# Kernel optimization log

Measured on AMD Instinct MI355X. Metric: run time of the kernel, lower is better.

The kernel has to match this reference:

```python
import jax, jax.numpy as jnp
import numpy as np
from jax import lax

DIM = 256; HEADS = 16; DHEAD = 16; H = 12; W = 26
DS = 4; KOFF = 6; OSCALE = 4.0
SCALE = DHEAD ** -0.5
EPS = 1e-5


def _create_grid(hh, ww, dtype):
    # channel0 = x (width index), channel1 = y (height index); matches torch meshgrid(arange(w), arange(h), indexing='xy')
    gy, gx = jnp.meshgrid(jnp.arange(hh, dtype=dtype), jnp.arange(ww, dtype=dtype), indexing='ij')
    return jnp.stack([gx, gy], axis=0)  # (2, hh, ww)


def _grid_sample_bilinear(img, grid):
    # F.grid_sample, mode='bilinear', padding_mode='zeros', align_corners=False
    # img (B,C,Hi,Wi); grid (B,Ho,Wo,2), grid[...,0]=x-norm, grid[...,1]=y-norm in [-1,1]
    B, C, Hi, Wi = img.shape
    x = ((grid[..., 0] + 1.0) * Wi - 1.0) / 2.0
    y = ((grid[..., 1] + 1.0) * Hi - 1.0) / 2.0
    x0 = jnp.floor(x); y0 = jnp.floor(y)

    def gather(xi, yi):
        valid = ((xi >= 0) & (xi < Wi) & (yi >= 0) & (yi < Hi)).astype(img.dtype)
        xc = jnp.clip(xi, 0, Wi - 1).astype(jnp.int32)
        yc = jnp.clip(yi, 0, Hi - 1).astype(jnp.int32)
        v = jax.vmap(lambda im, yy, xx: im[:, yy, xx])(img, yc, xc)  # (B,C,Ho,Wo)
        return v * valid[:, None]

    wx1 = (x - x0)[:, None]; wx0 = 1.0 - wx1
    wy1 = (y - y0)[:, None]; wy0 = 1.0 - wy1
    return (gather(x0, y0) * wy0 * wx0 + gather(x0 + 1.0, y0) * wy0 * wx1
            + gather(x0, y0 + 1.0) * wy1 * wx0 + gather(x0 + 1.0, y0 + 1.0) * wy1 * wx1)


def _forward(x, q, w_off_dw, b_off_dw, w_off_pw, wk, wv, w_out, b_out,
             cpb_w1, cpb_b1, cpb_w2, cpb_b2, cpb_w3, cpb_b3,
             conv1d_w, conv1d_b, ln_g, ln_b):
    b = x.shape[0]
    # faithful to torch: q.repeat(1,1,h*w).view(bs,1,dim,h,w).squeeze(1) == tile then reshape
    q_map = jnp.tile(q[:, 0, :], (1, H * W)).reshape(b, DIM, H, W)

    # to_offsets: depthwise Conv2d(k=6,s=4,p=1) -> GELU -> 1x1 conv (no bias) -> tanh -> *offset_scale
    t = lax.conv_general_dilated(q_map, w_off_dw, window_strides=(DS, DS),
                                 padding=[(1, 1), (1, 1)], feature_group_count=DIM,
                                 dimension_numbers=('NCHW', 'OIHW', 'NCHW'))
    t = jax.nn.gelu(t + b_off_dw[None, :, None, None], approximate=False)
    off = jnp.tanh(jnp.einsum('oc,bchw->bohw', w_off_pw, t)) * OSCALE  # (b,2,Hk,Wk)
    Hk, Wk = off.shape[-2], off.shape[-1]  # 3, 6

    gkv = _create_grid(Hk, Wk, x.dtype)
    vg0 = gkv[0] + off[:, 0]
    vg1 = gkv[1] + off[:, 1]
    # faithful repo normalize_grid: channel0 / (h-1), channel1 / (w-1)
    n0 = 2.0 * vg0 / max(Hk - 1, 1) - 1.0
    n1 = 2.0 * vg1 / max(Wk - 1, 1) - 1.0
    vgrid_scaled = jnp.stack([n0, n1], axis=-1)  # (b, Hk, Wk, 2)

    kv = _grid_sample_bilinear(x, vgrid_scaled)  # (b, DIM, Hk, Wk)
    k = jnp.einsum('oc,bchw->bohw', wk, kv)
    v = jnp.einsum('oc,bchw->bohw', wv, kv)

    qh = (q_map * SCALE).reshape(b, HEADS, DHEAD, H * W).transpose(0, 1, 3, 2)  # (b,h,i,d)
    kh = k.reshape(b, HEADS, DHEAD, Hk * Wk).transpose(0, 1, 3, 2)              # (b,h,j,d)
    vh = v.reshape(b, HEADS, DHEAD, Hk * Wk).transpose(0, 1, 3, 2)
    sim = jnp.einsum('bhid,bhjd->bhij', qh, kh)  # (b,16,312,18)

    # CPB relative position bias
    gq = _create_grid(H, W, x.dtype)
    gq0 = 2.0 * gq[0] / max(H - 1, 1) - 1.0
    gq1 = 2.0 * gq[1] / max(W - 1, 1) - 1.0
    grid_q = jnp.stack([gq0, gq1], axis=-1).reshape(1, H * W, 2)
    grid_kv = vgrid_scaled.reshape(b, Hk * Wk, 2)
    pos = grid_q[:, :, None, :] - grid_kv[:, None, :, :]       # (b,i,j,2)
    bias = jnp.sign(pos) * jnp.log(jnp.abs(pos) + 1.0)
    bias = jax.nn.relu(bias @ cpb_w1.T + cpb_b1)
    bias = jax.nn.relu(bias @ cpb_w2.T + cpb_b2)
    bias = bias @ cpb_w3.T + cpb_b3                             # (b,i,j,heads)
    sim = sim + bias.transpose(0, 3, 1, 2)

    attn = jax.nn.softmax(sim, axis=-1)  # dropout(0.1) identity in eval
    out = jnp.einsum('bhij,bhjd->bhid', attn, vh)               # (b,h,i,d)
    out = out.transpose(0, 1, 3, 2).reshape(b, DIM, H, W)        # 'b h (x y) d -> b (h d) x y'
    out = jnp.einsum('oc,bchw->bohw', w_out, out) + b_out[None, :, None, None]

    # SpatialCrossAttention tail: view -> permute -> Conv1d(312,1,1) -> residual -> LayerNorm
    tokens = out.reshape(b, DIM, H * W).transpose(0, 2, 1)       # (b,312,256)
    pooled = jnp.einsum('t,btc->bc', conv1d_w, tokens)[:, None, :] + conv1d_b[None, :, None]
    y = pooled + q
    mu = y.mean(-1, keepdims=True)
    var = y.var(-1, keepdims=True)
    return (y - mu) / jnp.sqrt(var + EPS) * ln_g + ln_b          # (b,1,256)


def setup_inputs() -> dict:
    key = jax.random.key(0)
    ks = jax.random.split(key, 16)
    rn = lambda i, shape, s=0.02: jax.random.normal(ks[i], shape, dtype=jnp.float32) * s
    B = 256
    return {
        'x': jax.random.normal(ks[0], (B, DIM, H, W), dtype=jnp.float32),
        'q': jax.random.normal(ks[1], (B, 1, DIM), dtype=jnp.float32),
        'w_off_dw': rn(2, (DIM, 1, KOFF, KOFF), 0.05),
        'b_off_dw': jnp.zeros((DIM,), jnp.float32),
        'w_off_pw': rn(3, (2, DIM), 0.05),
        'wk': rn(4, (DIM, DIM)),
        'wv': rn(5, (DIM, DIM)),
        'w_out': rn(6, (DIM, DIM)),
        'b_out': jnp.zeros((DIM,), jnp.float32),
        'cpb_w1': rn(7, (64, 2), 0.1),
        'cpb_b1': jnp.zeros((64,), jnp.float32),
        'cpb_w2': rn(8, (64, 64), 0.1),
        'cpb_b2': jnp.zeros((64,), jnp.float32),
        'cpb_w3': rn(9, (HEADS, 64), 0.1),
        'cpb_b3': jnp.zeros((HEADS,), jnp.float32),
        'conv1d_w': rn(10, (H * W,), 0.05),
        'conv1d_b': jnp.zeros((1,), jnp.float32),
        'ln_g': jnp.ones((DIM,), jnp.float32),
        'ln_b': jnp.zeros((DIM,), jnp.float32),
    }


def reference(x, q, w_off_dw, b_off_dw, w_off_pw, wk, wv, w_out, b_out,
              cpb_w1, cpb_b1, cpb_w2, cpb_b2, cpb_w3, cpb_b3,
              conv1d_w, conv1d_b, ln_g, ln_b):
    return _forward(x, q, w_off_dw, b_off_dw, w_off_pw, wk, wv, w_out, b_out,
                    cpb_w1, cpb_b1, cpb_w2, cpb_b2, cpb_w3, cpb_b3,
                    conv1d_w, conv1d_b, ln_g, ln_b)
```

## Files before the change

kernel.cpp:

```cpp
#include <hip/hip_runtime.h>
#include <hip/hip_bf16.h>
#include <math.h>


typedef __attribute__((ext_vector_type(8))) short short8;
typedef __attribute__((ext_vector_type(4))) float floatx4;

union U16 { uint4 u; short8 s; };

#define MFMA(A, B, C) __builtin_amdgcn_mfma_f32_16x16x32_bf16((A), (B), (C), 0, 0, 0)

__device__ __forceinline__ unsigned int f2bf(float f) {
    unsigned int u = __float_as_uint(f);
    u += 0x7fffu + ((u >> 16) & 1u);
    return u >> 16;
}
__device__ __forceinline__ unsigned int pk2(float a, float b) {
    __hip_bfloat162 h = __float22bfloat162_rn(make_float2(a, b));
    union { __hip_bfloat162 h; unsigned int u; } cv; cv.h = h;
    return cv.u;
}
__device__ __forceinline__ float bf2f(unsigned short v) {
    return __uint_as_float((unsigned int)v << 16);
}
__device__ __forceinline__ uint4 pack8(float4 a, float4 b) {
    uint4 r;
    r.x = pk2(a.x, a.y); r.y = pk2(a.z, a.w);
    r.z = pk2(b.x, b.y); r.w = pk2(b.z, b.w);
    return r;
}

__global__ __launch_bounds__(512, 2) void k_all(
    const float* __restrict__ x, const float* __restrict__ q,
    const float* __restrict__ w_dw, const float* __restrict__ b_dw,
    const float* __restrict__ w_pw,
    const float* __restrict__ wk, const float* __restrict__ wv,
    const float* __restrict__ w_out, const float* __restrict__ b_out,
    const float* __restrict__ cw1, const float* __restrict__ cb1,
    const float* __restrict__ cw2, const float* __restrict__ cb2,
    const float* __restrict__ cw3, const float* __restrict__ cb3,
    const float* __restrict__ conv_w, const float* __restrict__ conv_b,
    const float* __restrict__ ln_g, const float* __restrict__ ln_b,
    float* __restrict__ out)
{
    const int b = blockIdx.x, tid = threadIdx.x;
    const int w = tid >> 6, lane = tid & 63;
    const int n = lane & 15, qd = lane >> 4;

    __shared__ float qf_s[256];
    __shared__ unsigned short q_sb[256];
    __shared__ unsigned short v_sb[5120];
    __shared__ float F0[468], F1[216];
    __shared__ unsigned int lutxy[312];
    __shared__ float off_s[36], n0_s[18], n1_s[18];
    __shared__ float sx0[18], sy0[18], swx[18], swy[18];
    __shared__ float b2_s[64], b3_s[16];
    __shared__ float wA_s[288];
    __shared__ __align__(16) float m_s[256];
    __shared__ float pooled_s[256], redb[24];
    __shared__ __align__(16) unsigned char UB[113152];
    float* Sbuf = (float*)UB;
    unsigned short* kvT = (unsigned short*)UB;
    float* qsw = (float*)UB;
    float* t_s = (float*)(UB + 16512);
    unsigned short* k_sb = (unsigned short*)(UB + 16512);
    unsigned int* h2w = (unsigned int*)(UB + 78336);
    float* wred = (float*)UB;

    uint4 W2f[4][2], W3f[2];
    {
        const float4* cw2_4 = (const float4*)cw2;
        #pragma unroll
        for (int mtl = 0; mtl < 4; ++mtl)
            #pragma unroll
            for (int ks = 0; ks < 2; ++ks) {
                const int base = (mtl * 16 + n) * 16 + ks * 8 + qd * 2;
                W2f[mtl][ks] = pack8(cw2_4[base], cw2_4[base + 1]);
            }
        const float4* cw3_4 = (const float4*)cw3;
        #pragma unroll
        for (int ks = 0; ks < 2; ++ks) {
            const int base = n * 16 + ks * 8 + qd * 2;
            W3f[ks] = pack8(cw3_4[base], cw3_4[base + 1]);
        }
    }
    float W1a[16], W1b[16], B1r[16];
    #pragma unroll
    for (int kk = 0; kk < 16; ++kk) {
        const int kid = (kk < 8) ? (qd * 8 + kk) : (32 + qd * 8 + kk - 8);
        W1a[kk] = cw1[kid * 2]; W1b[kk] = cw1[kid * 2 + 1]; B1r[kk] = cb1[kid];
    }

    if (tid < 256) {
        const float qv = q[b * 256 + tid];
        qf_s[tid] = qv;
        q_sb[tid] = (unsigned short)f2bf(qv * 0.25f);
    }
    for (int u = tid; u < 4128; u += 512) {
        const int r = u / 258, i = u - r * 258;
        qsw[u] = (i < 256) ? q[b * 256 + i] : 0.f;
    }
    if (tid < 312) {
        const int iy = tid / 26;
        lutxy[tid] = (unsigned int)(tid - iy * 26) | ((unsigned int)iy << 16);
    }
    if (tid < 64) b2_s[tid] = cb2[tid];
    if (tid < 16) b3_s[tid] = cb3[tid];
    __syncthreads();

    {
        const int c = tid & 255, g = tid >> 8;
        float wreg[36];
        const float4* wdw4 = (const float4*)w_dw;
        #pragma unroll
        for (int i = 0; i < 9; ++i) {
            const float4 t4 = wdw4[c * 9 + i];
            wreg[i * 4 + 0] = t4.x; wreg[i * 4 + 1] = t4.y;
            wreg[i * 4 + 2] = t4.z; wreg[i * 4 + 3] = t4.w;
        }
        float acc[9];
        const float bv = b_dw[c];
        #pragma unroll
        for (int a = 0; a < 9; ++a) acc[a] = bv;
        const int cb = (c * 56) & 255;
        const int cp = (c & 15) * 258;
        for (int jh = 0; jh < 3; ++jh) {
            for (int kh = 0; kh < 6; ++kh) {
                const int ih = jh * 4 - 1 + kh;
                if (ih < 0 || ih >= 12) continue;
                const int rb = ih * 26;
                #pragma unroll
                for (int jwl = 0; jwl < 3; ++jwl) {
                    const int jw = g * 3 + jwl;
                    #pragma unroll
                    for (int kw = 0; kw < 6; ++kw) {
                        const int iw = jw * 4 - 1 + kw;
                        if (iw < 0 || iw >= 26) continue;
                        acc[jh * 3 + jwl] += wreg[kh * 6 + kw] * qsw[cp + ((cb + rb + iw) & 255)];
                    }
                }
            }
        }
        #pragma unroll
        for (int a = 0; a < 9; ++a) {
            const int jh = a / 3, jwl = a - jh * 3;
            const int p = jh * 6 + g * 3 + jwl;
            const float v = acc[a];
            t_s[p * 256 + c] = 0.5f * v * (1.0f + erff(v * 0.70710678118654752f));
        }
    }
    __syncthreads();

    for (int oi = w; oi < 36; oi += 8) {
        const int o = oi / 18, p = oi - o * 18;
        float s = 0.f;
        for (int c = lane; c < 256; c += 64) s += w_pw[o * 256 + c] * t_s[p * 256 + c];
        for (int d = 32; d > 0; d >>= 1) s += __shfl_down(s, d, 64);
        if (lane == 0) off_s[oi] = 4.0f * tanhf(s);
    }
    __syncthreads();

    if (tid < 18) {
        const int j = tid, jh = j / 6, jw = j - jh * 6;
        const float vg0 = (float)jw + off_s[j];
        const float vg1 = (float)jh + off_s[18 + j];
        const float n0 = 2.0f * vg0 / 2.0f - 1.0f;
        const float n1 = 2.0f * vg1 / 5.0f - 1.0f;
        n0_s[j] = n0; n1_s[j] = n1;
        const float xp = ((n0 + 1.0f) * 26.0f - 1.0f) * 0.5f;
        const float yp = ((n1 + 1.0f) * 12.0f - 1.0f) * 0.5f;
        const float x0 = floorf(xp), y0 = floorf(yp);
        sx0[j] = x0; sy0[j] = y0; swx[j] = xp - x0; swy[j] = yp - y0;
    }
    __syncthreads();

    {
        const int c = tid & 255, g = tid >> 8;
        const float* xb = x + ((size_t)b * 256 + c) * 312;
        for (int jj = 0; jj < 9; ++jj) {
            const int j = g * 9 + jj;
            const int x0 = (int)sx0[j], y0 = (int)sy0[j];
            const int x1 = x0 + 1, y1 = y0 + 1;
            const float wx1 = swx[j], wy1 = swy[j];
            const float wx0 = 1.f - wx1, wy0 = 1.f - wy1;
            const bool xv0 = (x0 >= 0) & (x0 < 26), xv1 = (x1 >= 0) & (x1 < 26);
            const bool yv0 = (y0 >= 0) & (y0 < 12), yv1 = (y1 >= 0) & (y1 < 12);
            const float v00 = (xv0 & yv0) ? xb[y0 * 26 + x0] : 0.f;
            const float v01 = (xv1 & yv0) ? xb[y0 * 26 + x1] : 0.f;
            const float v10 = (xv0 & yv1) ? xb[y1 * 26 + x0] : 0.f;
            const float v11 = (xv1 & yv1) ? xb[y1 * 26 + x1] : 0.f;
            const float val = wy0 * (wx0 * v00 + wx1 * v01) + wy1 * (wx0 * v10 + wx1 * v11);
            kvT[j * 264 + c] = (unsigned short)f2bf(val);
        }
    }
    for (int u = tid; u < 684; u += 512) {
        if (u < 468) {
            const int ixv = u / 18, j = u - ixv * 18;
            const float p0 = (float)ixv * (2.0f / 11.0f) - 1.0f - n0_s[j];
            F0[u] = copysignf(__logf(1.0f + fabsf(p0)), p0);
        } else {
            const int u2 = u - 468;
            const int iyv = u2 / 18, j = u2 - iyv * 18;
            const float p1 = (float)iyv * (2.0f / 25.0f) - 1.0f - n1_s[j];
            F1[u2] = copysignf(__logf(1.0f + fabsf(p1)), p1);
        }
    }
    __syncthreads();

    {
        const int m2 = w & 1, mtb = w >> 1;
        const float4* wm4 = (const float4*)(m2 ? wv : wk);
        floatx4 pa[4][2];
        #pragma unroll
        for (int a = 0; a < 4; ++a) {
            pa[a][0] = (floatx4){0.f, 0.f, 0.f, 0.f};
            pa[a][1] = (floatx4){0.f, 0.f, 0.f, 0.f};
        }
        #pragma unroll 2
        for (int ks = 0; ks < 8; ++ks) {
            U16 b0, b1;
            b0.u = *(const uint4*)(kvT + n * 264 + ks * 32 + qd * 8);
            b1.u = make_uint4(0u, 0u, 0u, 0u);
            if (n < 2) b1.u = *(const uint4*)(kvT + (16 + n) * 264 + ks * 32 + qd * 8);
            #pragma unroll
            for (int mtl = 0; mtl < 4; ++mtl) {
                const int mt = mtb + mtl * 4;
                const int f4i = (mt * 16 + n) * 64 + ks * 8 + qd * 2;
                U16 A; A.u = pack8(wm4[f4i], wm4[f4i + 1]);
                pa[mtl][0] = MFMA(A.s, b0.s, pa[mtl][0]);
                pa[mtl][1] = MFMA(A.s, b1.s, pa[mtl][1]);
            }
        }
        unsigned short* dst = m2 ? v_sb : k_sb;
        #pragma unroll
        for (int mtl = 0; mtl < 4; ++mtl) {
            const int mt = mtb + mtl * 4;
            #pragma unroll
            for (int r = 0; r < 4; ++r) {
                const int o = mt * 16 + qd * 4 + r;
                dst[o * 20 + n] = (unsigned short)f2bf(pa[mtl][0][r]);
                if (n < 2) dst[o * 20 + 16 + n] = (unsigned short)f2bf(pa[mtl][1][r]);
            }
        }
    }
    __syncthreads();

    uint4 BkU[2][2];
    #pragma unroll
    for (int hh = 0; hh < 2; ++hh)
        #pragma unroll
        for (int jt = 0; jt < 2; ++jt) {
            unsigned int u0 = 0, u1 = 0, u2 = 0, u3 = 0;
            if (qd < 2 && (jt == 0 || n < 2)) {
                const int h = w * 2 + hh;
                const int j = jt * 16 + n;
                const int cb0 = (h * 16 + qd * 8) * 20 + j;
                u0 = (unsigned)k_sb[cb0] | ((unsigned)k_sb[cb0 + 20] << 16);
                u1 = (unsigned)k_sb[cb0 + 40] | ((unsigned)k_sb[cb0 + 60] << 16);
                u2 = (unsigned)k_sb[cb0 + 80] | ((unsigned)k_sb[cb0 + 100] << 16);
                u3 = (unsigned)k_sb[cb0 + 120] | ((unsigned)k_sb[cb0 + 140] << 16);
            }
            BkU[hh][jt] = make_uint4(u0, u1, u2, u3);
        }
    __syncthreads();

    float wAcc[18];
    #pragma unroll
    for (int j = 0; j < 18; ++j) wAcc[j] = 0.f;

    auto soft_acc = [&](int chp, const float* Sp) {
        const int il = tid >> 4, h = tid & 15;
        const int CIp = (chp == 9) ? 24 : 32;
        if (il < CIp) {
            const float cwv = conv_w[chp * 32 + il];
            float lv[18];
            #pragma unroll
            for (int j = 0; j < 18; ++j) lv[j] = Sp[(il * 18 + j) * 17 + h];
            float m = lv[0];
            #pragma unroll
            for (int j = 1; j < 18; ++j) m = fmaxf(m, lv[j]);
            float s = 0.f;
            #pragma unroll
            for (int j = 0; j < 18; ++j) { lv[j] = __expf(lv[j] - m); s += lv[j]; }
            const float wgt = cwv / s;
            #pragma unroll
            for (int j = 0; j < 18; ++j) wAcc[j] = fmaf(wgt, lv[j], wAcc[j]);
        }
    };

    for (int ch = 0; ch < 10; ++ch) {
        float* Sc = Sbuf + (ch & 1) * 9792;
        const float* Sp = Sbuf + ((ch & 1) ^ 1) * 9792;
        const int ibase = ch * 32;

        #pragma unroll
        for (int hh = 0; hh < 2; ++hh) {
            const int h = w * 2 + hh;
            const int base = h * 16 + qd * 8;
            #pragma unroll
            for (int ig = 0; ig < 2; ++ig) {
                unsigned int a0 = 0, a1 = 0, a2 = 0, a3u = 0;
                if (qd < 2) {
                    const int ii = ibase + ig * 16 + n;
                    a0 = (unsigned)q_sb[((base + 0) * 56 + ii) & 255] |
                         ((unsigned)q_sb[((base + 1) * 56 + ii) & 255] << 16);
                    a1 = (unsigned)q_sb[((base + 2) * 56 + ii) & 255] |
                         ((unsigned)q_sb[((base + 3) * 56 + ii) & 255] << 16);
                    a2 = (unsigned)q_sb[((base + 4) * 56 + ii) & 255] |
                         ((unsigned)q_sb[((base + 5) * 56 + ii) & 255] << 16);
                    a3u = (unsigned)q_sb[((base + 6) * 56 + ii) & 255] |
                          ((unsigned)q_sb[((base + 7) * 56 + ii) & 255] << 16);
                }
                U16 Af; Af.u = make_uint4(a0, a1, a2, a3u);
                #pragma unroll
                for (int jt = 0; jt < 2; ++jt) {
                    U16 Bf; Bf.u = BkU[hh][jt];
                    floatx4 D = {0.f, 0.f, 0.f, 0.f};
                    D = MFMA(Af.s, Bf.s, D);
                    const int j = jt * 16 + n;
                    if (j < 18) {
                        #pragma unroll
                        for (int r = 0; r < 4; ++r)
                            Sc[((ig * 16 + qd * 4 + r) * 18 + j) * 17 + h] = D[r];
                    }
                }
            }
        }
        if (ch > 0) soft_acc(ch - 1, Sp);
        __syncthreads();

        {
            auto mlp2 = [&](int tA, int tB, bool two) {
                const int tv2[2] = {tA, tB};
                U16 ub0[2], ub1[2];
                #pragma unroll
                for (int u2 = 0; u2 < 2; ++u2) {
                    const int t = tv2[u2];
                    const int ig = (t >= 18) ? 1 : 0;
                    const int j = t - ig * 18;
                    const int i0 = ibase + ig * 16 + n;
                    const unsigned int lv2 = lutxy[(i0 < 312) ? i0 : 311];
                    const int ix = (int)(lv2 & 0xffffu), iy = (int)(lv2 >> 16);
                    const float f0 = F0[ix * 18 + j];
                    const float f1 = F1[iy * 18 + j];
                    unsigned int uu[8];
                    #pragma unroll
                    for (int kp = 0; kp < 8; ++kp) {
                        const float ha = fmaxf(fmaf(W1a[2*kp],   f0, fmaf(W1b[2*kp],   f1, B1r[2*kp])),   0.f);
                        const float hb = fmaxf(fmaf(W1a[2*kp+1], f0, fmaf(W1b[2*kp+1], f1, B1r[2*kp+1])), 0.f);
                        uu[kp] = pk2(ha, hb);
                    }
                    ub0[u2].u = make_uint4(uu[0], uu[1], uu[2], uu[3]);
                    ub1[u2].u = make_uint4(uu[4], uu[5], uu[6], uu[7]);
                }
                #pragma unroll
                for (int u2 = 0; u2 < 2; ++u2) {
                    if (u2 == 1 && !two) break;
                    unsigned int* hw = h2w + ((w << 1) | u2) * 544 + n * 34;
                    #pragma unroll
                    for (int mtl = 0; mtl < 4; ++mtl) {
                        U16 A0, A1; A0.u = W2f[mtl][0]; A1.u = W2f[mtl][1];
                        floatx4 acc = {0.f, 0.f, 0.f, 0.f};
                        acc = MFMA(A0.s, ub0[u2].s, acc);
                        acc = MFMA(A1.s, ub1[u2].s, acc);
                        const float e0 = fmaxf(acc[0] + b2_s[mtl*16 + qd*4 + 0], 0.f);
                        const float e1 = fmaxf(acc[1] + b2_s[mtl*16 + qd*4 + 1], 0.f);
                        const float e2 = fmaxf(acc[2] + b2_s[mtl*16 + qd*4 + 2], 0.f);
                        const float e3 = fmaxf(acc[3] + b2_s[mtl*16 + qd*4 + 3], 0.f);
                        hw[mtl * 8 + qd * 2]     = pk2(e0, e1);
                        hw[mtl * 8 + qd * 2 + 1] = pk2(e2, e3);
                    }
                }
                #pragma unroll
                for (int u2 = 0; u2 < 2; ++u2) {
                    if (u2 == 1 && !two) break;
                    const unsigned int* hwr = h2w + ((w << 1) | u2) * 544;
                    U16 uc0, uc1;
                    uc0.u = *(const uint4*)(hwr + n * 34 + qd * 4);
                    uc1.u = *(const uint4*)(hwr + n * 34 + 16 + qd * 4);
                    U16 A0, A1; A0.u = W3f[0]; A1.u = W3f[1];
                    floatx4 a3 = {0.f, 0.f, 0.f, 0.f};
                    a3 = MFMA(A0.s, uc0.s, a3);
                    a3 = MFMA(A1.s, uc1.s, a3);
                    const int t = tv2[u2];
                    const int ig = (t >= 18) ? 1 : 0;
                    const int j = t - ig * 18;
                    float* sp = Sc + ((ig * 16 + n) * 18 + j) * 17 + qd * 4;
                    #pragma unroll
                    for (int r = 0; r < 4; ++r) sp[r] = a3[r] + b3_s[qd * 4 + r] + sp[r];
                }
            };
            mlp2(w, w + 8, true);
            mlp2(w + 16, w + 24, true);
            if (w < 4) mlp2(32 + w, 32 + w, false);
        }
        __syncthreads();
    }
    soft_acc(9, Sbuf + 9792);

    #pragma unroll
    for (int j = 0; j < 18; ++j) wred[tid * 18 + j] = wAcc[j];
    {
        float v = 0.f;
        for (int u = tid; u < 312; u += 512) v += conv_w[u];
        for (int d = 32; d > 0; d >>= 1) v += __shfl_down(v, d, 64);
        if (lane == 0) redb[w] = v;
    }
    __syncthreads();
    for (int u = tid; u < 288; u += 512) {
        const int h = u / 18, j = u - h * 18;
        float s = 0.f;
        #pragma unroll
        for (int sl = 0; sl < 32; ++sl) s += wred[(sl * 16 + h) * 18 + j];
        wA_s[u] = s;
    }
    __syncthreads();

    if (tid < 256) {
        const int hb = (tid >> 4) * 18;
        float acc = 0.f;
        #pragma unroll
        for (int j = 0; j < 18; ++j) acc += wA_s[hb + j] * bf2f(v_sb[tid * 20 + j]);
        m_s[tid] = acc;
    }
    __syncthreads();

    float Ssum = 0.f;
    #pragma unroll
    for (int i = 0; i < 8; ++i) Ssum += redb[i];

    {
        const float4 mm = *(const float4*)(m_s + lane * 4);
        for (int ol = 0; ol < 32; ++ol) {
            const int o = w * 32 + ol;
            const float4 wq = *(const float4*)(w_out + o * 256 + lane * 4);
            float d = wq.x * mm.x + wq.y * mm.y + wq.z * mm.z + wq.w * mm.w;
            for (int dd = 32; dd > 0; dd >>= 1) d += __shfl_down(d, dd, 64);
            if (lane == 0) pooled_s[o] = d;
        }
    }
    __syncthreads();

    if (tid < 256) {
        const float y = pooled_s[tid] + b_out[tid] * Ssum + conv_b[0] + qf_s[tid];
        float s1 = y, s2 = y * y;
        for (int d = 32; d > 0; d >>= 1) { s1 += __shfl_down(s1, d, 64); s2 += __shfl_down(s2, d, 64); }
        if (lane == 0) { redb[16 + w] = s1; redb[20 + w] = s2; }
    }
    __syncthreads();
    if (tid < 256) {
        const float y = pooled_s[tid] + b_out[tid] * Ssum + conv_b[0] + qf_s[tid];
        const float S1 = redb[16] + redb[17] + redb[18] + redb[19];
        const float S2 = redb[20] + redb[21] + redb[22] + redb[23];
        const float mu = S1 * (1.0f / 256.0f);
        const float var = S2 * (1.0f / 256.0f) - mu * mu;
        out[b * 256 + tid] = (y - mu) * rsqrtf(var + 1e-5f) * ln_g[tid] + ln_b[tid];
    }
}

extern "C" void kernel_launch(void* const* d_in, const int* in_sizes, int n_in,
                              void* d_out, int out_size, void* d_ws, size_t ws_size,
                              hipStream_t stream) {
    const float* x       = (const float*)d_in[0];
    const float* q       = (const float*)d_in[1];
    const float* w_dw    = (const float*)d_in[2];
    const float* b_dwp   = (const float*)d_in[3];
    const float* w_pw    = (const float*)d_in[4];
    const float* wk      = (const float*)d_in[5];
    const float* wv      = (const float*)d_in[6];
    const float* w_out   = (const float*)d_in[7];
    const float* b_out   = (const float*)d_in[8];
    const float* cw1     = (const float*)d_in[9];
    const float* cb1     = (const float*)d_in[10];
    const float* cw2     = (const float*)d_in[11];
    const float* cb2     = (const float*)d_in[12];
    const float* cw3     = (const float*)d_in[13];
    const float* cb3     = (const float*)d_in[14];
    const float* conv_w  = (const float*)d_in[15];
    const float* conv_b  = (const float*)d_in[16];
    const float* ln_g    = (const float*)d_in[17];
    const float* ln_b    = (const float*)d_in[18];
    float* out = (float*)d_out;

    k_all<<<256, 512, 0, stream>>>(x, q, w_dw, b_dwp, w_pw, wk, wv, w_out, b_out,
                                   cw1, cb1, cw2, cb2, cw3, cb3,
                                   conv_w, conv_b, ln_g, ln_b, out);
}
```

Before: 261.2 us.

## Double block size to 1024 threads and redistribute per-wave work

Launches 1024 threads per block instead of 512 and re-splits every phase: depthwise conv positions, grid sampling, K/V projection tiles, one head per wave in the score MFMA, single-token MLP per call, and softmax split across two lanes with shuffle reductions. It also moves the MLP weight register loads to later in the kernel, which shortens their live range. The goal is more waves per block to hide latency and fewer serial iterations per thread. The cost is one block per CU instead of two, plus extra shuffles and barrier cost across more waves.

```diff
diff --git a/kernel.cpp b/kernel.cpp
--- a/kernel.cpp
+++ b/kernel.cpp
@@ -30,7 +30,7 @@
     return r;
 }
 
-__global__ __launch_bounds__(512, 2) void k_all(
+__global__ __launch_bounds__(1024, 1) void k_all(
     const float* __restrict__ x, const float* __restrict__ q,
     const float* __restrict__ w_dw, const float* __restrict__ b_dw,
     const float* __restrict__ w_pw,
@@ -67,36 +67,12 @@
     unsigned int* h2w = (unsigned int*)(UB + 78336);
     float* wred = (float*)UB;
 
-    uint4 W2f[4][2], W3f[2];
-    {
-        const float4* cw2_4 = (const float4*)cw2;
-        #pragma unroll
-        for (int mtl = 0; mtl < 4; ++mtl)
-            #pragma unroll
-            for (int ks = 0; ks < 2; ++ks) {
-                const int base = (mtl * 16 + n) * 16 + ks * 8 + qd * 2;
-                W2f[mtl][ks] = pack8(cw2_4[base], cw2_4[base + 1]);
-            }
-        const float4* cw3_4 = (const float4*)cw3;
-        #pragma unroll
-        for (int ks = 0; ks < 2; ++ks) {
-            const int base = n * 16 + ks * 8 + qd * 2;
-            W3f[ks] = pack8(cw3_4[base], cw3_4[base + 1]);
-        }
-    }
-    float W1a[16], W1b[16], B1r[16];
-    #pragma unroll
-    for (int kk = 0; kk < 16; ++kk) {
-        const int kid = (kk < 8) ? (qd * 8 + kk) : (32 + qd * 8 + kk - 8);
-        W1a[kk] = cw1[kid * 2]; W1b[kk] = cw1[kid * 2 + 1]; B1r[kk] = cb1[kid];
-    }
-
     if (tid < 256) {
         const float qv = q[b * 256 + tid];
         qf_s[tid] = qv;
         q_sb[tid] = (unsigned short)f2bf(qv * 0.25f);
     }
-    for (int u = tid; u < 4128; u += 512) {
+    for (int u = tid; u < 4128; u += 1024) {
         const int r = u / 258, i = u - r * 258;
         qsw[u] = (i < 256) ? q[b * 256 + i] : 0.f;
     }
@@ -118,40 +94,35 @@
             wreg[i * 4 + 0] = t4.x; wreg[i * 4 + 1] = t4.y;
             wreg[i * 4 + 2] = t4.z; wreg[i * 4 + 3] = t4.w;
         }
-        float acc[9];
         const float bv = b_dw[c];
-        #pragma unroll
-        for (int a = 0; a < 9; ++a) acc[a] = bv;
         const int cb = (c * 56) & 255;
         const int cp = (c & 15) * 258;
-        for (int jh = 0; jh < 3; ++jh) {
-            for (int kh = 0; kh < 6; ++kh) {
-                const int ih = jh * 4 - 1 + kh;
-                if (ih < 0 || ih >= 12) continue;
-                const int rb = ih * 26;
+        #pragma unroll
+        for (int it = 0; it < 5; ++it) {
+            const int p = g + it * 4;
+            if (p < 18) {
+                const int jh = (p >= 12) ? 2 : ((p >= 6) ? 1 : 0);
+                const int jw = p - jh * 6;
+                float acc = bv;
                 #pragma unroll
-                for (int jwl = 0; jwl < 3; ++jwl) {
-                    const int jw = g * 3 + jwl;
+                for (int kh = 0; kh < 6; ++kh) {
+                    const int ih = jh * 4 - 1 + kh;
+                    if (ih < 0 || ih >= 12) continue;
+                    const int rb = ih * 26;
                     #pragma unroll
                     for (int kw = 0; kw < 6; ++kw) {
                         const int iw = jw * 4 - 1 + kw;
                         if (iw < 0 || iw >= 26) continue;
-                        acc[jh * 3 + jwl] += wreg[kh * 6 + kw] * qsw[cp + ((cb + rb + iw) & 255)];
+                        acc += wreg[kh * 6 + kw] * qsw[cp + ((cb + rb + iw) & 255)];
                     }
                 }
-            }
-        }
-        #pragma unroll
-        for (int a = 0; a < 9; ++a) {
-            const int jh = a / 3, jwl = a - jh * 3;
-            const int p = jh * 6 + g * 3 + jwl;
-            const float v = acc[a];
-            t_s[p * 256 + c] = 0.5f * v * (1.0f + erff(v * 0.70710678118654752f));
-        }
-    }
-    __syncthreads();
-
-    for (int oi = w; oi < 36; oi += 8) {
+                t_s[p * 256 + c] = 0.5f * acc * (1.0f + erff(acc * 0.70710678118654752f));
+            }
+        }
+    }
+    __syncthreads();
+
+    for (int oi = w; oi < 36; oi += 16) {
         const int o = oi / 18, p = oi - o * 18;
         float s = 0.f;
         for (int c = lane; c < 256; c += 64) s += w_pw[o * 256 + c] * t_s[p * 256 + c];
@@ -177,23 +148,26 @@
     {
         const int c = tid & 255, g = tid >> 8;
         const float* xb = x + ((size_t)b * 256 + c) * 312;
-        for (int jj = 0; jj < 9; ++jj) {
-            const int j = g * 9 + jj;
-            const int x0 = (int)sx0[j], y0 = (int)sy0[j];
-            const int x1 = x0 + 1, y1 = y0 + 1;
-            const float wx1 = swx[j], wy1 = swy[j];
-            const float wx0 = 1.f - wx1, wy0 = 1.f - wy1;
-            const bool xv0 = (x0 >= 0) & (x0 < 26), xv1 = (x1 >= 0) & (x1 < 26);
-            const bool yv0 = (y0 >= 0) & (y0 < 12), yv1 = (y1 >= 0) & (y1 < 12);
-            const float v00 = (xv0 & yv0) ? xb[y0 * 26 + x0] : 0.f;
-            const float v01 = (xv1 & yv0) ? xb[y0 * 26 + x1] : 0.f;
-            const float v10 = (xv0 & yv1) ? xb[y1 * 26 + x0] : 0.f;
-            const float v11 = (xv1 & yv1) ? xb[y1 * 26 + x1] : 0.f;
-            const float val = wy0 * (wx0 * v00 + wx1 * v01) + wy1 * (wx0 * v10 + wx1 * v11);
-            kvT[j * 264 + c] = (unsigned short)f2bf(val);
-        }
-    }
-    for (int u = tid; u < 684; u += 512) {
+        #pragma unroll
+        for (int jj = 0; jj < 5; ++jj) {
+            const int j = g + jj * 4;
+            if (j < 18) {
+                const int x0 = (int)sx0[j], y0 = (int)sy0[j];
+                const int x1 = x0 + 1, y1 = y0 + 1;
+                const float wx1 = swx[j], wy1 = swy[j];
+                const float wx0 = 1.f - wx1, wy0 = 1.f - wy1;
+                const bool xv0 = (x0 >= 0) & (x0 < 26), xv1 = (x1 >= 0) & (x1 < 26);
+                const bool yv0 = (y0 >= 0) & (y0 < 12), yv1 = (y1 >= 0) & (y1 < 12);
+                const float v00 = (xv0 & yv0) ? xb[y0 * 26 + x0] : 0.f;
+                const float v01 = (xv1 & yv0) ? xb[y0 * 26 + x1] : 0.f;
+                const float v10 = (xv0 & yv1) ? xb[y1 * 26 + x0] : 0.f;
+                const float v11 = (xv1 & yv1) ? xb[y1 * 26 + x1] : 0.f;
+                const float val = wy0 * (wx0 * v00 + wx1 * v01) + wy1 * (wx0 * v10 + wx1 * v11);
+                kvT[j * 264 + c] = (unsigned short)f2bf(val);
+            }
+        }
+    }
+    for (int u = tid; u < 684; u += 1024) {
         if (u < 468) {
             const int ixv = u / 18, j = u - ixv * 18;
             const float p0 = (float)ixv * (2.0f / 11.0f) - 1.0f - n0_s[j];
@@ -210,9 +184,9 @@
     {
         const int m2 = w & 1, mtb = w >> 1;
         const float4* wm4 = (const float4*)(m2 ? wv : wk);
-        floatx4 pa[4][2];
-        #pragma unroll
-        for (int a = 0; a < 4; ++a) {
+        floatx4 pa[2][2];
+        #pragma unroll
+        for (int a = 0; a < 2; ++a) {
             pa[a][0] = (floatx4){0.f, 0.f, 0.f, 0.f};
             pa[a][1] = (floatx4){0.f, 0.f, 0.f, 0.f};
         }
@@ -223,8 +197,8 @@
             b1.u = make_uint4(0u, 0u, 0u, 0u);
             if (n < 2) b1.u = *(const uint4*)(kvT + (16 + n) * 264 + ks * 32 + qd * 8);
             #pragma unroll
-            for (int mtl = 0; mtl < 4; ++mtl) {
-                const int mt = mtb + mtl * 4;
+            for (int mtl = 0; mtl < 2; ++mtl) {
+                const int mt = mtb + mtl * 8;
                 const int f4i = (mt * 16 + n) * 64 + ks * 8 + qd * 2;
                 U16 A; A.u = pack8(wm4[f4i], wm4[f4i + 1]);
                 pa[mtl][0] = MFMA(A.s, b0.s, pa[mtl][0]);
@@ -233,8 +207,8 @@
         }
         unsigned short* dst = m2 ? v_sb : k_sb;
         #pragma unroll
-        for (int mtl = 0; mtl < 4; ++mtl) {
-            const int mt = mtb + mtl * 4;
+        for (int mtl = 0; mtl < 2; ++mtl) {
+            const int mt = mtb + mtl * 8;
             #pragma unroll
             for (int r = 0; r < 4; ++r) {
                 const int o = mt * 16 + qd * 4 + r;
@@ -245,46 +219,70 @@
     }
     __syncthreads();
 
-    uint4 BkU[2][2];
+    uint4 W2f[4][2], W3f[2];
+    {
+        const float4* cw2_4 = (const float4*)cw2;
+        #pragma unroll
+        for (int mtl = 0; mtl < 4; ++mtl)
+            #pragma unroll
+            for (int ks = 0; ks < 2; ++ks) {
+                const int base = (mtl * 16 + n) * 16 + ks * 8 + qd * 2;
+                W2f[mtl][ks] = pack8(cw2_4[base], cw2_4[base + 1]);
+            }
+        const float4* cw3_4 = (const float4*)cw3;
+        #pragma unroll
+        for (int ks = 0; ks < 2; ++ks) {
+            const int base = n * 16 + ks * 8 + qd * 2;
+            W3f[ks] = pack8(cw3_4[base], cw3_4[base + 1]);
+        }
+    }
+    float W1a[16], W1b[16], B1r[16];
     #pragma unroll
-    for (int hh = 0; hh < 2; ++hh)
-        #pragma unroll
-        for (int jt = 0; jt < 2; ++jt) {
-            unsigned int u0 = 0, u1 = 0, u2 = 0, u3 = 0;
-            if (qd < 2 && (jt == 0 || n < 2)) {
-                const int h = w * 2 + hh;
-                const int j = jt * 16 + n;
-                const int cb0 = (h * 16 + qd * 8) * 20 + j;
-                u0 = (unsigned)k_sb[cb0] | ((unsigned)k_sb[cb0 + 20] << 16);
-                u1 = (unsigned)k_sb[cb0 + 40] | ((unsigned)k_sb[cb0 + 60] << 16);
-                u2 = (unsigned)k_sb[cb0 + 80] | ((unsigned)k_sb[cb0 + 100] << 16);
-                u3 = (unsigned)k_sb[cb0 + 120] | ((unsigned)k_sb[cb0 + 140] << 16);
-            }
-            BkU[hh][jt] = make_uint4(u0, u1, u2, u3);
-        }
-    __syncthreads();
-
-    float wAcc[18];
+    for (int kk = 0; kk < 16; ++kk) {
+        const int kid = (kk < 8) ? (qd * 8 + kk) : (32 + qd * 8 + kk - 8);
+        W1a[kk] = cw1[kid * 2]; W1b[kk] = cw1[kid * 2 + 1]; B1r[kk] = cb1[kid];
+    }
+
+    uint4 BkU[2];
     #pragma unroll
-    for (int j = 0; j < 18; ++j) wAcc[j] = 0.f;
+    for (int jt = 0; jt < 2; ++jt) {
+        unsigned int u0 = 0, u1 = 0, u2 = 0, u3 = 0;
+        if (qd < 2 && (jt == 0 || n < 2)) {
+            const int j = jt * 16 + n;
+            const int cb0 = (w * 16 + qd * 8) * 20 + j;
+            u0 = (unsigned)k_sb[cb0] | ((unsigned)k_sb[cb0 + 20] << 16);
+            u1 = (unsigned)k_sb[cb0 + 40] | ((unsigned)k_sb[cb0 + 60] << 16);
+            u2 = (unsigned)k_sb[cb0 + 80] | ((unsigned)k_sb[cb0 + 100] << 16);
+            u3 = (unsigned)k_sb[cb0 + 120] | ((unsigned)k_sb[cb0 + 140] << 16);
+        }
+        BkU[jt] = make_uint4(u0, u1, u2, u3);
+    }
+    __syncthreads();
+
+    float wAcc[9];
+    #pragma unroll
+    for (int jl = 0; jl < 9; ++jl) wAcc[jl] = 0.f;
 
     auto soft_acc = [&](int chp, const float* Sp) {
-        const int il = tid >> 4, h = tid & 15;
+        const int h = tid & 15, hf = (tid >> 4) & 1, il = tid >> 5;
         const int CIp = (chp == 9) ? 24 : 32;
         if (il < CIp) {
             const float cwv = conv_w[chp * 32 + il];
-            float lv[18];
-            #pragma unroll
-            for (int j = 0; j < 18; ++j) lv[j] = Sp[(il * 18 + j) * 17 + h];
+            float lv[9];
+            const float* row = Sp + (il * 18 + hf * 9) * 17 + h;
+            #pragma unroll
+            for (int jl = 0; jl < 9; ++jl) lv[jl] = row[jl * 17];
             float m = lv[0];
             #pragma unroll
-            for (int j = 1; j < 18; ++j) m = fmaxf(m, lv[j]);
+            for (int jl = 1; jl < 9; ++jl) m = fmaxf(m, lv[jl]);
+            m = fmaxf(m, __shfl_xor(m, 16, 64));
             float s = 0.f;
             #pragma unroll
-            for (int j = 0; j < 18; ++j) { lv[j] = __expf(lv[j] - m); s += lv[j]; }
+            for (int jl = 0; jl < 9; ++jl) { lv[jl] = __expf(lv[jl] - m); s += lv[jl]; }
+            s += __shfl_xor(s, 16, 64);
             const float wgt = cwv / s;
             #pragma unroll
-            for (int j = 0; j < 18; ++j) wAcc[j] = fmaf(wgt, lv[j], wAcc[j]);
+            for (int jl = 0; jl < 9; ++jl) wAcc[jl] = fmaf(wgt, lv[jl], wAcc[jl]);
         }
     };
 
@@ -293,10 +291,8 @@
         const float* Sp = Sbuf + ((ch & 1) ^ 1) * 9792;
         const int ibase = ch * 32;
 
-        #pragma unroll
-        for (int hh = 0; hh < 2; ++hh) {
-            const int h = w * 2 + hh;
-            const int base = h * 16 + qd * 8;
+        {
+            const int base = w * 16 + qd * 8;
             #pragma unroll
             for (int ig = 0; ig < 2; ++ig) {
                 unsigned int a0 = 0, a1 = 0, a2 = 0, a3u = 0;
@@ -314,14 +310,14 @@
                 U16 Af; Af.u = make_uint4(a0, a1, a2, a3u);
                 #pragma unroll
                 for (int jt = 0; jt < 2; ++jt) {
-                    U16 Bf; Bf.u = BkU[hh][jt];
+                    U16 Bf; Bf.u = BkU[jt];
                     floatx4 D = {0.f, 0.f, 0.f, 0.f};
                     D = MFMA(Af.s, Bf.s, D);
                     const int j = jt * 16 + n;
                     if (j < 18) {
                         #pragma unroll
                         for (int r = 0; r < 4; ++r)
-                            Sc[((ig * 16 + qd * 4 + r) * 18 + j) * 17 + h] = D[r];
+                            Sc[((ig * 16 + qd * 4 + r) * 18 + j) * 17 + w] = D[r];
                     }
                 }
             }
@@ -330,19 +326,16 @@
         __syncthreads();
 
         {
-            auto mlp2 = [&](int tA, int tB, bool two) {
-                const int tv2[2] = {tA, tB};
-                U16 ub0[2], ub1[2];
-                #pragma unroll
-                for (int u2 = 0; u2 < 2; ++u2) {
-                    const int t = tv2[u2];
-                    const int ig = (t >= 18) ? 1 : 0;
-                    const int j = t - ig * 18;
-                    const int i0 = ibase + ig * 16 + n;
-                    const unsigned int lv2 = lutxy[(i0 < 312) ? i0 : 311];
-                    const int ix = (int)(lv2 & 0xffffu), iy = (int)(lv2 >> 16);
-                    const float f0 = F0[ix * 18 + j];
-                    const float f1 = F1[iy * 18 + j];
+            auto mlp1 = [&](int t) {
+                const int ig = (t >= 18) ? 1 : 0;
+                const int j = t - ig * 18;
+                const int i0 = ibase + ig * 16 + n;
+                const unsigned int lv2 = lutxy[(i0 < 312) ? i0 : 311];
+                const int ix = (int)(lv2 & 0xffffu), iy = (int)(lv2 >> 16);
+                const float f0 = F0[ix * 18 + j];
+                const float f1 = F1[iy * 18 + j];
+                U16 ub0, ub1;
+                {
                     unsigned int uu[8];
                     #pragma unroll
                     for (int kp = 0; kp < 8; ++kp) {
@@ -350,69 +343,59 @@
                         const float hb = fmaxf(fmaf(W1a[2*kp+1], f0, fmaf(W1b[2*kp+1], f1, B1r[2*kp+1])), 0.f);
                         uu[kp] = pk2(ha, hb);
                     }
-                    ub0[u2].u = make_uint4(uu[0], uu[1], uu[2], uu[3]);
-                    ub1[u2].u = make_uint4(uu[4], uu[5], uu[6], uu[7]);
+                    ub0.u = make_uint4(uu[0], uu[1], uu[2], uu[3]);
+                    ub1.u = make_uint4(uu[4], uu[5], uu[6], uu[7]);
                 }
+                unsigned int* hw = h2w + w * 544 + n * 34;
                 #pragma unroll
-                for (int u2 = 0; u2 < 2; ++u2) {
-                    if (u2 == 1 && !two) break;
-                    unsigned int* hw = h2w + ((w << 1) | u2) * 544 + n * 34;
-                    #pragma unroll
-                    for (int mtl = 0; mtl < 4; ++mtl) {
-                        U16 A0, A1; A0.u = W2f[mtl][0]; A1.u = W2f[mtl][1];
-                        floatx4 acc = {0.f, 0.f, 0.f, 0.f};
-                        acc = MFMA(A0.s, ub0[u2].s, acc);
-                        acc = MFMA(A1.s, ub1[u2].s, acc);
-                        const float e0 = fmaxf(acc[0] + b2_s[mtl*16 + qd*4 + 0], 0.f);
-                        const float e1 = fmaxf(acc[1] + b2_s[mtl*16 + qd*4 + 1], 0.f);
-                        const float e2 = fmaxf(acc[2] + b2_s[mtl*16 + qd*4 + 2], 0.f);
-                        const float e3 = fmaxf(acc[3] + b2_s[mtl*16 + qd*4 + 3], 0.f);
-                        hw[mtl * 8 + qd * 2]     = pk2(e0, e1);
-                        hw[mtl * 8 + qd * 2 + 1] = pk2(e2, e3);
-                    }
+                for (int mtl = 0; mtl < 4; ++mtl) {
+                    U16 A0, A1; A0.u = W2f[mtl][0]; A1.u = W2f[mtl][1];
+                    floatx4 acc = {0.f, 0.f, 0.f, 0.f};
+                    acc = MFMA(A0.s, ub0.s, acc);
+                    acc = MFMA(A1.s, ub1.s, acc);
+                    const float e0 = fmaxf(acc[0] + b2_s[mtl*16 + qd*4 + 0], 0.f);
+                    const float e1 = fmaxf(acc[1] + b2_s[mtl*16 + qd*4 + 1], 0.f);
+                    const float e2 = fmaxf(acc[2] + b2_s[mtl*16 + qd*4 + 2], 0.f);
+                    const float e3 = fmaxf(acc[3] + b2_s[mtl*16 + qd*4 + 3], 0.f);
+                    hw[mtl * 8 + qd * 2]     = pk2(e0, e1);
+                    hw[mtl * 8 + qd * 2 + 1] = pk2(e2, e3);
                 }
+                const unsigned int* hwr = h2w + w * 544;
+                U16 uc0, uc1;
+                uc0.u = *(const uint4*)(hwr + n * 34 + qd * 4);
+                uc1.u = *(const uint4*)(hwr + n * 34 + 16 + qd * 4);
+                U16 A0, A1; A0.u = W3f[0]; A1.u = W3f[1];
+                floatx4 a3 = {0.f, 0.f, 0.f, 0.f};
+                a3 = MFMA(A0.s, uc0.s, a3);
+                a3 = MFMA(A1.s, uc1.s, a3);
+                float* sp = Sc + ((ig * 16 + n) * 18 + j) * 17 + qd * 4;
                 #pragma unroll
-                for (int u2 = 0; u2 < 2; ++u2) {
-                    if (u2 == 1 && !two) break;
-                    const unsigned int* hwr = h2w + ((w << 1) | u2) * 544;
-                    U16 uc0, uc1;
-                    uc0.u = *(const uint4*)(hwr + n * 34 + qd * 4);
-                    uc1.u = *(const uint4*)(hwr + n * 34 + 16 + qd * 4);
-                    U16 A0, A1; A0.u = W3f[0]; A1.u = W3f[1];
-                    floatx4 a3 = {0.f, 0.f, 0.f, 0.f};
-                    a3 = MFMA(A0.s, uc0.s, a3);
-                    a3 = MFMA(A1.s, uc1.s, a3);
-                    const int t = tv2[u2];
-                    const int ig = (t >= 18) ? 1 : 0;
-                    const int j = t - ig * 18;
-                    float* sp = Sc + ((ig * 16 + n) * 18 + j) * 17 + qd * 4;
-                    #pragma unroll
-                    for (int r = 0; r < 4; ++r) sp[r] = a3[r] + b3_s[qd * 4 + r] + sp[r];
-                }
+                for (int r = 0; r < 4; ++r) sp[r] = a3[r] + b3_s[qd * 4 + r] + sp[r];
             };
-            mlp2(w, w + 8, true);
-            mlp2(w + 16, w + 24, true);
-            if (w < 4) mlp2(32 + w, 32 + w, false);
+            mlp1(w);
+            mlp1(w + 16);
+            if (w < 4) mlp1(32 + w);
         }
         __syncthreads();
     }
     soft_acc(9, Sbuf + 9792);
 
     #pragma unroll
-    for (int j = 0; j < 18; ++j) wred[tid * 18 + j] = wAcc[j];
+    for (int jl = 0; jl < 9; ++jl) wred[tid * 9 + jl] = wAcc[jl];
     {
         float v = 0.f;
-        for (int u = tid; u < 312; u += 512) v += conv_w[u];
+        for (int u = tid; u < 312; u += 1024) v += conv_w[u];
         for (int d = 32; d > 0; d >>= 1) v += __shfl_down(v, d, 64);
         if (lane == 0) redb[w] = v;
     }
     __syncthreads();
-    for (int u = tid; u < 288; u += 512) {
-        const int h = u / 18, j = u - h * 18;
+    if (tid < 288) {
+        const int h = tid / 18, j2 = tid - h * 18;
+        const int hf = (j2 >= 9) ? 1 : 0, jl = j2 - hf * 9;
         float s = 0.f;
         #pragma unroll
-        for (int sl = 0; sl < 32; ++sl) s += wred[(sl * 16 + h) * 18 + j];
-        wA_s[u] = s;
+        for (int sl = 0; sl < 32; ++sl) s += wred[(sl * 32 + hf * 16 + h) * 9 + jl];
+        wA_s[tid] = s;
     }
     __syncthreads();
 
@@ -427,12 +410,12 @@
 
     float Ssum = 0.f;
     #pragma unroll
-    for (int i = 0; i < 8; ++i) Ssum += redb[i];
+    for (int i = 0; i < 16; ++i) Ssum += redb[i];
 
     {
         const float4 mm = *(const float4*)(m_s + lane * 4);
-        for (int ol = 0; ol < 32; ++ol) {
-            const int o = w * 32 + ol;
+        for (int ol = 0; ol < 16; ++ol) {
+            const int o = w * 16 + ol;
             const float4 wq = *(const float4*)(w_out + o * 256 + lane * 4);
             float d = wq.x * mm.x + wq.y * mm.y + wq.z * mm.z + wq.w * mm.w;
             for (int dd = 32; dd > 0; dd >>= 1) d += __shfl_down(d, dd, 64);
@@ -482,7 +465,7 @@
     const float* ln_b    = (const float*)d_in[18];
     float* out = (float*)d_out;
 
-    k_all<<<256, 512, 0, stream>>>(x, q, w_dw, b_dwp, w_pw, wk, wv, w_out, b_out,
-                                   cw1, cb1, cw2, cb2, cw3, cb3,
-                                   conv_w, conv_b, ln_g, ln_b, out);
-}
+    k_all<<<256, 1024, 0, stream>>>(x, q, w_dw, b_dwp, w_pw, wk, wv, w_out, b_out,
+                                    cw1, cb1, cw2, cb2, cw3, cb3,
+                                    conv_w, conv_b, ln_g, ln_b, out);
+}
```

Result: slower. 382.5 us (+46.5%).

## Pipeline score, MLP bias and softmax stages over triple-buffered chunks

Applied to the files above, without the earlier changes.

Restructures the per-chunk loop into a three-stage software pipeline (QK MFMA, CPB MLP bias add, softmax accumulation) using three score buffers, so each iteration needs only one barrier instead of two. The first-layer MLP weights move from per-thread registers into a packed shared table, and the W2/W3 fragment loads are deferred until after the projection phase, both to reduce register pressure. The MLP now processes one position at a time with a single h2w scratch per wave. Shared memory grows to hold the third buffer, which may limit occupancy, and the MLP loses its two-position batching.

```diff
diff --git a/kernel.cpp b/kernel.cpp
--- a/kernel.cpp
+++ b/kernel.cpp
@@ -55,41 +55,18 @@
     __shared__ float off_s[36], n0_s[18], n1_s[18];
     __shared__ float sx0[18], sy0[18], swx[18], swy[18];
     __shared__ float b2_s[64], b3_s[16];
+    __shared__ __align__(16) float w1p[4][8][8];
     __shared__ float wA_s[288];
     __shared__ __align__(16) float m_s[256];
     __shared__ float pooled_s[256], redb[24];
-    __shared__ __align__(16) unsigned char UB[113152];
+    __shared__ __align__(16) unsigned char UB[134912];
     float* Sbuf = (float*)UB;
     unsigned short* kvT = (unsigned short*)UB;
     float* qsw = (float*)UB;
     float* t_s = (float*)(UB + 16512);
     unsigned short* k_sb = (unsigned short*)(UB + 16512);
-    unsigned int* h2w = (unsigned int*)(UB + 78336);
-    float* wred = (float*)UB;
-
-    uint4 W2f[4][2], W3f[2];
-    {
-        const float4* cw2_4 = (const float4*)cw2;
-        #pragma unroll
-        for (int mtl = 0; mtl < 4; ++mtl)
-            #pragma unroll
-            for (int ks = 0; ks < 2; ++ks) {
-                const int base = (mtl * 16 + n) * 16 + ks * 8 + qd * 2;
-                W2f[mtl][ks] = pack8(cw2_4[base], cw2_4[base + 1]);
-            }
-        const float4* cw3_4 = (const float4*)cw3;
-        #pragma unroll
-        for (int ks = 0; ks < 2; ++ks) {
-            const int base = n * 16 + ks * 8 + qd * 2;
-            W3f[ks] = pack8(cw3_4[base], cw3_4[base + 1]);
-        }
-    }
-    float W1a[16], W1b[16], B1r[16];
-    #pragma unroll
-    for (int kk = 0; kk < 16; ++kk) {
-        const int kid = (kk < 8) ? (qd * 8 + kk) : (32 + qd * 8 + kk - 8);
-        W1a[kk] = cw1[kid * 2]; W1b[kk] = cw1[kid * 2 + 1]; B1r[kk] = cb1[kid];
-    }
+    unsigned int* h2w = (unsigned int*)(UB + 117504);
+    float* wred = (float*)(UB + 39168);
 
     if (tid < 256) {
         const float qv = q[b * 256 + tid];
@@ -106,6 +83,19 @@
     }
     if (tid < 64) b2_s[tid] = cb2[tid];
     if (tid < 16) b3_s[tid] = cb3[tid];
+    if (tid >= 64 && tid < 96) {
+        const int t2 = tid - 64;
+        const int qdi = t2 >> 3, kp = t2 & 7;
+        const int kk0 = 2 * kp, kk1 = 2 * kp + 1;
+        const int kid0 = (kk0 < 8) ? (qdi * 8 + kk0) : (32 + qdi * 8 + kk0 - 8);
+        const int kid1 = (kk1 < 8) ? (qdi * 8 + kk1) : (32 + qdi * 8 + kk1 - 8);
+        w1p[qdi][kp][0] = cw1[kid0 * 2];
+        w1p[qdi][kp][1] = cw1[kid0 * 2 + 1];
+        w1p[qdi][kp][2] = cb1[kid0];
+        w1p[qdi][kp][3] = cw1[kid1 * 2];
+        w1p[qdi][kp][4] = cw1[kid1 * 2 + 1];
+        w1p[qdi][kp][5] = cb1[kid1];
+    }
     __syncthreads();
 
     {
@@ -245,6 +235,24 @@
     }
     __syncthreads();
 
+    uint4 W2f[4][2], W3f[2];
+    {
+        const float4* cw2_4 = (const float4*)cw2;
+        #pragma unroll
+        for (int mtl = 0; mtl < 4; ++mtl)
+            #pragma unroll
+            for (int ks = 0; ks < 2; ++ks) {
+                const int base = (mtl * 16 + n) * 16 + ks * 8 + qd * 2;
+                W2f[mtl][ks] = pack8(cw2_4[base], cw2_4[base + 1]);
+            }
+        const float4* cw3_4 = (const float4*)cw3;
+        #pragma unroll
+        for (int ks = 0; ks < 2; ++ks) {
+            const int base = n * 16 + ks * 8 + qd * 2;
+            W3f[ks] = pack8(cw3_4[base], cw3_4[base + 1]);
+        }
+    }
+
     uint4 BkU[2][2];
     #pragma unroll
     for (int hh = 0; hh < 2; ++hh)
@@ -274,8 +282,9 @@
         if (il < CIp) {
             const float cwv = conv_w[chp * 32 + il];
             float lv[18];
-            #pragma unroll
-            for (int j = 0; j < 18; ++j) lv[j] = Sp[(il * 18 + j) * 17 + h];
+            const float* row = Sp + (il * 18) * 17 + h;
+            #pragma unroll
+            for (int j = 0; j < 18; ++j) lv[j] = row[j * 17];
             float m = lv[0];
             #pragma unroll
             for (int j = 1; j < 18; ++j) m = fmaxf(m, lv[j]);
@@ -288,115 +297,104 @@
         }
     };
 
-    for (int ch = 0; ch < 10; ++ch) {
-        float* Sc = Sbuf + (ch & 1) * 9792;
-        const float* Sp = Sbuf + ((ch & 1) ^ 1) * 9792;
-        const int ibase = ch * 32;
-
-        #pragma unroll
-        for (int hh = 0; hh < 2; ++hh) {
-            const int h = w * 2 + hh;
-            const int base = h * 16 + qd * 8;
-            #pragma unroll
-            for (int ig = 0; ig < 2; ++ig) {
-                unsigned int a0 = 0, a1 = 0, a2 = 0, a3u = 0;
-                if (qd < 2) {
-                    const int ii = ibase + ig * 16 + n;
-                    a0 = (unsigned)q_sb[((base + 0) * 56 + ii) & 255] |
-                         ((unsigned)q_sb[((base + 1) * 56 + ii) & 255] << 16);
-                    a1 = (unsigned)q_sb[((base + 2) * 56 + ii) & 255] |
-                         ((unsigned)q_sb[((base + 3) * 56 + ii) & 255] << 16);
-                    a2 = (unsigned)q_sb[((base + 4) * 56 + ii) & 255] |
-                         ((unsigned)q_sb[((base + 5) * 56 + ii) & 255] << 16);
-                    a3u = (unsigned)q_sb[((base + 6) * 56 + ii) & 255] |
-                          ((unsigned)q_sb[((base + 7) * 56 + ii) & 255] << 16);
-                }
-                U16 Af; Af.u = make_uint4(a0, a1, a2, a3u);
+    for (int t = 0; t < 12; ++t) {
+        if (t < 10) {
+            float* Sc = Sbuf + (t % 3) * 9792;
+            const int ibase = t * 32;
+            #pragma unroll
+            for (int hh = 0; hh < 2; ++hh) {
+                const int h = w * 2 + hh;
+                const int base = h * 16 + qd * 8;
                 #pragma unroll
-                for (int jt = 0; jt < 2; ++jt) {
-                    U16 Bf; Bf.u = BkU[hh][jt];
-                    floatx4 D = {0.f, 0.f, 0.f, 0.f};
-                    D = MFMA(Af.s, Bf.s, D);
-                    const int j = jt * 16 + n;
-                    if (j < 18) {
-                        #pragma unroll
-                        for (int r = 0; r < 4; ++r)
-                            Sc[((ig * 16 + qd * 4 + r) * 18 + j) * 17 + h] = D[r];
+                for (int ig = 0; ig < 2; ++ig) {
+                    unsigned int a0 = 0, a1 = 0, a2 = 0, a3u = 0;
+                    if (qd < 2) {
+                        const int ii = ibase + ig * 16 + n;
+                        a0 = (unsigned)q_sb[((base + 0) * 56 + ii) & 255] |
+                             ((unsigned)q_sb[((base + 1) * 56 + ii) & 255] << 16);
+                        a1 = (unsigned)q_sb[((base + 2) * 56 + ii) & 255] |
+                             ((unsigned)q_sb[((base + 3) * 56 + ii) & 255] << 16);
+                        a2 = (unsigned)q_sb[((base + 4) * 56 + ii) & 255] |
+                             ((unsigned)q_sb[((base + 5) * 56 + ii) & 255] << 16);
+                        a3u = (unsigned)q_sb[((base + 6) * 56 + ii) & 255] |
+                              ((unsigned)q_sb[((base + 7) * 56 + ii) & 255] << 16);
+                    }
+                    U16 Af; Af.u = make_uint4(a0, a1, a2, a3u);
+                    #pragma unroll
+                    for (int jt = 0; jt < 2; ++jt) {
+                        U16 Bf; Bf.u = BkU[hh][jt];
+                        floatx4 D = {0.f, 0.f, 0.f, 0.f};
+                        D = MFMA(Af.s, Bf.s, D);
+                        const int j = jt * 16 + n;
+                        if (j < 18) {
+                            #pragma unroll
+                            for (int r = 0; r < 4; ++r)
+                                Sc[((ig * 16 + qd * 4 + r) * 18 + j) * 17 + h] = D[r];
+                        }
                     }
                 }
             }
         }
-        if (ch > 0) soft_acc(ch - 1, Sp);
-        __syncthreads();
-
-        {
-            auto mlp2 = [&](int tA, int tB, bool two) {
-                const int tv2[2] = {tA, tB};
-                U16 ub0[2], ub1[2];
-                #pragma unroll
-                for (int u2 = 0; u2 < 2; ++u2) {
-                    const int t = tv2[u2];
-                    const int ig = (t >= 18) ? 1 : 0;
-                    const int j = t - ig * 18;
-                    const int i0 = ibase + ig * 16 + n;
-                    const unsigned int lv2 = lutxy[(i0 < 312) ? i0 : 311];
-                    const int ix = (int)(lv2 & 0xffffu), iy = (int)(lv2 >> 16);
-                    const float f0 = F0[ix * 18 + j];
-                    const float f1 = F1[iy * 18 + j];
+        if (t >= 1 && t < 11) {
+            const int chm = t - 1;
+            float* Sm = Sbuf + (chm % 3) * 9792;
+            const int ibase = chm * 32;
+            auto mlp1 = [&](int tt) {
+                const int ig = (tt >= 18) ? 1 : 0;
+                const int j = tt - ig * 18;
+                const int i0 = ibase + ig * 16 + n;
+                const unsigned int lv2 = lutxy[(i0 < 312) ? i0 : 311];
+                const int ix = (int)(lv2 & 0xffffu), iy = (int)(lv2 >> 16);
+                const float f0 = F0[ix * 18 + j];
+                const float f1 = F1[iy * 18 + j];
+                U16 ub0, ub1;
+                {
                     unsigned int uu[8];
                     #pragma unroll
                     for (int kp = 0; kp < 8; ++kp) {
-                        const float ha = fmaxf(fmaf(W1a[2*kp],   f0, fmaf(W1b[2*kp],   f1, B1r[2*kp])),   0.f);
-                        const float hb = fmaxf(fmaf(W1a[2*kp+1], f0, fmaf(W1b[2*kp+1], f1, B1r[2*kp+1])), 0.f);
+                        const float* wp = &w1p[qd][kp][0];
+                        const float ha = fmaxf(fmaf(wp[0], f0, fmaf(wp[1], f1, wp[2])), 0.f);
+                        const float hb = fmaxf(fmaf(wp[3], f0, fmaf(wp[4], f1, wp[5])), 0.f);
                         uu[kp] = pk2(ha, hb);
                     }
-                    ub0[u2].u = make_uint4(uu[0], uu[1], uu[2], uu[3]);
-                    ub1[u2].u = make_uint4(uu[4], uu[5], uu[6], uu[7]);
+                    ub0.u = make_uint4(uu[0], uu[1], uu[2], uu[3]);
+                    ub1.u = make_uint4(uu[4], uu[5], uu[6], uu[7]);
                 }
+                unsigned int* hw = h2w + w * 544 + n * 34;
                 #pragma unroll
-                for (int u2 = 0; u2 < 2; ++u2) {
-                    if (u2 == 1 && !two) break;
-                    unsigned int* hw = h2w + ((w << 1) | u2) * 544 + n * 34;
-                    #pragma unroll
-                    for (int mtl = 0; mtl < 4; ++mtl) {
-                        U16 A0, A1; A0.u = W2f[mtl][0]; A1.u = W2f[mtl][1];
-                        floatx4 acc = {0.f, 0.f, 0.f, 0.f};
-                        acc = MFMA(A0.s, ub0[u2].s, acc);
-                        acc = MFMA(A1.s, ub1[u2].s, acc);
-                        const float e0 = fmaxf(acc[0] + b2_s[mtl*16 + qd*4 + 0], 0.f);
-                        const float e1 = fmaxf(acc[1] + b2_s[mtl*16 + qd*4 + 1], 0.f);
-                        const float e2 = fmaxf(acc[2] + b2_s[mtl*16 + qd*4 + 2], 0.f);
-                        const float e3 = fmaxf(acc[3] + b2_s[mtl*16 + qd*4 + 3], 0.f);
-                        hw[mtl * 8 + qd * 2]     = pk2(e0, e1);
-                        hw[mtl * 8 + qd * 2 + 1] = pk2(e2, e3);
-                    }
+                for (int mtl = 0; mtl < 4; ++mtl) {
+                    U16 A0, A1; A0.u = W2f[mtl][0]; A1.u = W2f[mtl][1];
+                    floatx4 acc = {0.f, 0.f, 0.f, 0.f};
+                    acc = MFMA(A0.s, ub0.s, acc);
+                    acc = MFMA(A1.s, ub1.s, acc);
+                    const float e0 = fmaxf(acc[0] + b2_s[mtl*16 + qd*4 + 0], 0.f);
+                    const float e1 = fmaxf(acc[1] + b2_s[mtl*16 + qd*4 + 1], 0.f);
+                    const float e2 = fmaxf(acc[2] + b2_s[mtl*16 + qd*4 + 2], 0.f);
+                    const float e3 = fmaxf(acc[3] + b2_s[mtl*16 + qd*4 + 3], 0.f);
+                    hw[mtl * 8 + qd * 2]     = pk2(e0, e1);
+                    hw[mtl * 8 + qd * 2 + 1] = pk2(e2, e3);
                 }
+                const unsigned int* hwr = h2w + w * 544;
+                U16 uc0, uc1;
+                uc0.u = *(const uint4*)(hwr + n * 34 + qd * 4);
+                uc1.u = *(const uint4*)(hwr + n * 34 + 16 + qd * 4);
+                U16 A0, A1; A0.u = W3f[0]; A1.u = W3f[1];
+                floatx4 a3 = {0.f, 0.f, 0.f, 0.f};
+                a3 = MFMA(A0.s, uc0.s, a3);
+                a3 = MFMA(A1.s, uc1.s, a3);
+                float* sp = Sm + ((ig * 16 + n) * 18 + j) * 17 + qd * 4;
                 #pragma unroll
-                for (int u2 = 0; u2 < 2; ++u2) {
-                    if (u2 == 1 && !two) break;
-                    const unsigned int* hwr = h2w + ((w << 1) | u2) * 544;
-                    U16 uc0, uc1;
-                    uc0.u = *(const uint4*)(hwr + n * 34 + qd * 4);
-                    uc1.u = *(const uint4*)(hwr + n * 34 + 16 + qd * 4);
-                    U16 A0, A1; A0.u = W3f[0]; A1.u = W3f[1];
-                    floatx4 a3 = {0.f, 0.f, 0.f, 0.f};
-                    a3 = MFMA(A0.s, uc0.s, a3);
-                    a3 = MFMA(A1.s, uc1.s, a3);
-                    const int t = tv2[u2];
-                    const int ig = (t >= 18) ? 1 : 0;
-                    const int j = t - ig * 18;
-                    float* sp = Sc + ((ig * 16 + n) * 18 + j) * 17 + qd * 4;
-                    #pragma unroll
-                    for (int r = 0; r < 4; ++r) sp[r] = a3[r] + b3_s[qd * 4 + r] + sp[r];
-                }
+                for (int r = 0; r < 4; ++r) sp[r] = a3[r] + b3_s[qd * 4 + r] + sp[r];
             };
-            mlp2(w, w + 8, true);
-            mlp2(w + 16, w + 24, true);
-            if (w < 4) mlp2(32 + w, 32 + w, false);
-        }
+            mlp1(w);
+            mlp1(w + 8);
+            mlp1(w + 16);
+            mlp1(w + 24);
+            if (w < 4) mlp1(32 + w);
+        }
+        if (t >= 2) soft_acc(t - 2, Sbuf + ((t - 2) % 3) * 9792);
         __syncthreads();
     }
-    soft_acc(9, Sbuf + 9792);
 
     #pragma unroll
     for (int j = 0; j < 18; ++j) wred[tid * 18 + j] = wAcc[j];
```

After: 259.1 us. Within noise of the previous version (-0.8%).
